# Kernel optimization log

Hardware: AMD Instinct MI355X
Metric: run time of the kernel (lower is better)

Reference implementation:

```python
import jax, jax.numpy as jnp
import numpy as np

B, L, C = 8, 256, 64
NEG = -1e30  # large negative instead of -inf to keep grads NaN-free


def setup_inputs() -> dict:
    key = jax.random.key(0)
    k1, k2 = jax.random.split(key)
    scores = jax.random.normal(k1, (B, L, L, C), dtype=jnp.float32)
    lens = jax.random.randint(k2, (B,), 64, L, dtype=jnp.int32)  # sentence lengths in [64, L-1]
    return {"scores": scores, "lens": lens}


def _inside_max(scores, lens):
    """Max-semiring CKY inside pass. scores: [B,L,L,C]; returns logZ per batch [B]."""
    t = jnp.transpose(jnp.max(scores, axis=-1), (1, 2, 0))  # [L,L,B] best label per span
    s0 = jnp.zeros((L, L, B), scores.dtype)                 # chart s[i,j] = best score of span (i,j)
    i = jnp.arange(L)
    j = jnp.arange(L)

    def step(s, w):
        e = jnp.clip(i + w, 0, L - 1)                       # span end, [L]
        k = jnp.clip(i[:, None] + j[None, :], 0, L - 1)     # split points, [L,L]
        left = s[i[:, None], k]                             # s[i, i+j], [L,L,B]
        right = s[k, e[:, None]]                            # s[i+j, i+w], [L,L,B]
        valid = (j[None, :] >= 1) & (j[None, :] < w) & ((i + w) < L)[:, None]
        comb = jnp.max(jnp.where(valid[..., None], left + right, NEG), axis=1)  # [L,B]
        s_l = t[i, e]                                       # label-max span score, [L,B]
        diag = jnp.where(w == 1, s_l, comb + s_l)
        row_ok = ((i + w) < L)[:, None]
        upd = jnp.where(row_ok, diag, s[i, e])
        s = s.at[i, e].set(upd)
        return s, None

    s, _ = jax.lax.scan(step, s0, jnp.arange(1, L))
    lens_c = jnp.clip(lens, 1, L - 1)
    return s[0, lens_c, jnp.arange(B)]                      # logZ (best tree score) per sentence


def reference(scores, lens):
    return _inside_max(scores, lens)
```

## Files before the change

kernel.cpp:

```cpp
#include <hip/hip_runtime.h>

#define LVAL 256
#define T    32
#define ST   36
#define SLAB (T * ST)
#define NB   8
#define NEG  (-1e30f)

typedef float f32x4 __attribute__((ext_vector_type(4)));

#define SOFT_FENCE() asm volatile("" ::: "memory")

__device__ __forceinline__ size_t sidx(int b, int i, int e) {
    return ((size_t)b << 16) + (i << 8) + e;
}

__device__ __forceinline__ void st_coh4(float* p, f32x4 v) {
    asm volatile("global_store_dwordx4 %0, %1, off sc0 sc1"
                 :: "v"(p), "v"(v) : "memory");
}
__device__ __forceinline__ f32x4 ld_coh4(const float* p) {
    f32x4 v;
    asm volatile("global_load_dwordx4 %0, %1, off sc0 sc1\n\t"
                 "s_waitcnt vmcnt(0)"
                 : "=&v"(v) : "v"(p) : "memory");
    return v;
}
__device__ __forceinline__ void ld_coh4x4(const float* p,
                                          f32x4& a, f32x4& b, f32x4& c, f32x4& d) {
    asm volatile("global_load_dwordx4 %0, %4, off sc0 sc1\n\t"
                 "global_load_dwordx4 %1, %4, off offset:16 sc0 sc1\n\t"
                 "global_load_dwordx4 %2, %4, off offset:32 sc0 sc1\n\t"
                 "global_load_dwordx4 %3, %4, off offset:48 sc0 sc1\n\t"
                 "s_waitcnt vmcnt(0)"
                 : "=&v"(a), "=&v"(b), "=&v"(c), "=&v"(d)
                 : "v"(p) : "memory");
}

template<int CTRL>
__device__ __forceinline__ float dpp_max(float v) {
#if __has_builtin(__builtin_amdgcn_mov_dpp)
    int o = __builtin_amdgcn_mov_dpp(__builtin_bit_cast(int, v), CTRL, 0xF, 0xF, true);
    return fmaxf(v, __builtin_bit_cast(float, o));
#else
    return fmaxf(v, __shfl_xor(v, CTRL == 0xB1 ? 1 : 2));
#endif
}

__global__ __launch_bounds__(256) void phase1(const float* __restrict__ scores,
                                              float* __restrict__ s,
                                              int* __restrict__ bar) {
    if (blockIdx.x == 0 && blockIdx.y == 0) {
        for (int k = threadIdx.x; k < 2048; k += 256) bar[k] = 0;
    }
    const int i = blockIdx.x, b = blockIdx.y;
    const int sub = threadIdx.x & 15, slot = threadIdx.x >> 4;
    const float* row = scores + ((((size_t)b * LVAL + i) * LVAL) << 6);
    #pragma unroll 4
    for (int m0 = 0; m0 < LVAL; m0 += 16) {
        const int e = m0 + slot;
        if (e > i) {
            float4 v = *((const float4*)(row + ((size_t)e << 6)) + sub);
            float mx = fmaxf(fmaxf(v.x, v.y), fmaxf(v.z, v.w));
            #pragma unroll
            for (int d = 1; d < 16; d <<= 1) mx = fmaxf(mx, __shfl_xor(mx, d));
            if (sub == 0) s[sidx(b, i, e)] = mx;
        }
    }
}

template<int LP>
__device__ __forceinline__ void diag_step(int lane, int l,
                                          float (*cur)[ST], float (*curT)[ST],
                                          const float (*tb)[ST]) {
    const int cells = T - l;
    const int P = 1 << LP;
    const int c = lane >> LP, p = lane & (P - 1);
    const bool guard = c < cells;
    const int li = guard ? c : 0;
    const int le = guard ? c + l : 0;
    constexpr int NF = 8 >> LP;
    const float tv = tb[li][le];
    float acc = NEG;
    #pragma unroll
    for (int m = 0; m < NF; ++m) {
        const int k0 = 4 * (p + m * P);
        float4 cu = *(const float4*)&cur[li][k0];
        float4 ct = *(const float4*)&curT[le][k0];
        acc = fmaxf(acc, fmaxf(fmaxf(cu.x + ct.x, cu.y + ct.y),
                               fmaxf(cu.z + ct.z, cu.w + ct.w)));
    }
    acc = dpp_max<0xB1>(acc);
    if (LP >= 2) acc = dpp_max<0x4E>(acc);
    const float v = acc + tv;
    if (guard && p == 0) cur[li][le] = v;
    if (guard && p == 1) curT[le][li] = v;
}

template<int LP>
__device__ __forceinline__ void edge_step(int lane, int l, int D,
                                          const float (*Ae)[ST], const float (*BeT)[ST],
                                          float (*cur)[ST], float (*curT)[ST],
                                          const float (*tb)[ST], const float (*pre)[ST]) {
    const int delta = l - (T - 1);
    const int ad = delta < 0 ? -delta : delta;
    const int cells = T - ad;
    const int P = 1 << LP;
    const int c = lane >> LP, p = lane & (P - 1);
    const bool guard = c < cells;
    const int li = guard ? (delta < 0 ? c + ad : c) : 0;
    const int le = guard ? li + delta : 0;
    constexpr int NF = 8 >> LP;
    const float tv = tb[li][le];
    float acc = pre[li][le];
    #pragma unroll
    for (int m = 0; m < NF; ++m) {
        const int k0 = 4 * (p + m * P);
        float4 a  = *(const float4*)&Ae[li][k0];
        float4 ct = *(const float4*)&curT[le][k0];
        float4 cu = *(const float4*)&cur[li][k0];
        float4 bt = *(const float4*)&BeT[le][k0];
        float s0 = fmaxf(fmaxf(a.x + ct.x, a.y + ct.y), fmaxf(a.z + ct.z, a.w + ct.w));
        float s1 = fmaxf(fmaxf(cu.x + bt.x, cu.y + bt.y), fmaxf(cu.z + bt.z, cu.w + bt.w));
        acc = fmaxf(acc, fmaxf(s0, s1));
    }
    acc = dpp_max<0xB1>(acc);
    if (LP >= 2) acc = dpp_max<0x4E>(acc);
    const float v = (D == 1 && l == 0) ? tv : acc + tv;
    if (guard && p == 0) cur[li][le] = v;
    if (guard && p == 1) curT[le][li] = v;
}

__device__ __forceinline__ void batch_barrier(int* __restrict__ bar, int b,
                                              int tid, int ep) {
    asm volatile("s_waitcnt vmcnt(0)" ::: "memory");
    __syncthreads();
    if (tid == 0) {
        int* cnt  = bar + b * 256;
        int* flag = bar + b * 256 + 64;
        int prev = __hip_atomic_fetch_add(cnt, 1, __ATOMIC_RELAXED,
                                          __HIP_MEMORY_SCOPE_AGENT);
        if ((prev & (NB - 1)) == NB - 1) {
            __hip_atomic_store(flag, ep, __ATOMIC_RELAXED, __HIP_MEMORY_SCOPE_AGENT);
        } else {
            int guard = 0;
            while (__hip_atomic_load(flag, __ATOMIC_RELAXED,
                                     __HIP_MEMORY_SCOPE_AGENT) < ep) {
                __builtin_amdgcn_s_sleep(2);
                if (++guard > (1 << 22)) break;
            }
        }
    }
    __syncthreads();
}

__global__ __launch_bounds__(256) void dp_fused(float* __restrict__ s,
                                                const int* __restrict__ lens,
                                                float* __restrict__ out,
                                                int* __restrict__ bar) {
    __shared__ __align__(16) float smem[14 * SLAB];
    float* ATb = smem;
    float (*Ae)[ST]  = (float(*)[ST])(smem + 6 * SLAB);
    float (*tb)[ST]  = (float(*)[ST])(smem + 7 * SLAB);
    float (*BeT)[ST] = (float(*)[ST])(smem + 8 * SLAB);
    float (*cur)[ST] = (float(*)[ST])(smem + 9 * SLAB);
    float* BWb = smem + 10 * SLAB;
    float (*pre)[ST] = (float(*)[ST])BWb;

    const int b  = blockIdx.x & 7;
    const int bi = blockIdx.x >> 3;
    const int tid = threadIdx.x, wid = tid >> 6, lane = tid & 63;
    const int lr = tid >> 5, lc = tid & 31;
    const int grow = lane >> 1, gc = (lane & 1) * 16;
    const int gly = lane >> 3, glx = lane & 7, r0 = 4 * gly, c0 = 4 * glx;
    const int trow = tid >> 3, tc4 = (tid & 7) * 4;
    float (*BW)[ST] = (float(*)[ST])(BWb + wid * SLAB);

    if (wid == 0) {
        float (*curT0)[ST] = (float(*)[ST])(BWb + 1 * SLAB);
        float (*t0)[ST]    = (float(*)[ST])(BWb + 2 * SLAB);
        const float4 negv = make_float4(NEG, NEG, NEG, NEG);
        #pragma unroll
        for (int j = 0; j < 4; ++j) {
            float4 v = *(const float4*)&s[sidx(b, bi * T + grow, bi * T + gc + 4 * j)];
            *(float4*)&t0[grow][gc + 4 * j]    = v;
            *(float4*)&Ae[grow][gc + 4 * j]    = negv;
            *(float4*)&curT0[grow][gc + 4 * j] = negv;
        }
        SOFT_FENCE();
        if (lane < T - 1) {
            float v = t0[lane][lane + 1];
            Ae[lane][lane + 1] = v;
            curT0[lane + 1][lane] = v;
        }
        SOFT_FENCE();
        #pragma unroll 1
        for (int l = 2; l < T; ++l) {
            if (T - l <= 16) diag_step<2>(lane, l, Ae, curT0, t0);
            else             diag_step<1>(lane, l, Ae, curT0, t0);
            SOFT_FENCE();
        }
        #pragma unroll
        for (int j = 0; j < 4; ++j)
            st_coh4(&s[sidx(b, bi * T + grow, bi * T + gc + 4 * j)],
                    *(const f32x4*)&Ae[grow][gc + 4 * j]);
    } else if (bi + 1 < NB) {
        for (int idx = tid - 64; idx < 256; idx += 192) {
            const int row = idx >> 3, c4 = (idx & 7) * 4;
            *(float4*)&tb[row][c4] =
                *(const float4*)&s[sidx(b, bi * T + row, (bi + 1) * T + c4)];
        }
    }

    #pragma unroll 1
    for (int D = 1; D < NB; ++D) {
        batch_barrier(bar, b, tid, D);
        const int be = bi + D;
        if (be < NB) {
            if (D == 1) {
                f32x4 v = ld_coh4(&s[sidx(b, be * T + trow, be * T + tc4)]);
                BeT[tc4 + 0][trow] = (trow < tc4 + 0) ? v[0] : NEG;
                BeT[tc4 + 1][trow] = (trow < tc4 + 1) ? v[1] : NEG;
                BeT[tc4 + 2][trow] = (trow < tc4 + 2) ? v[2] : NEG;
                BeT[tc4 + 3][trow] = (trow < tc4 + 3) ? v[3] : NEG;
            }
            const int nw = (D - 1 < 4) ? (D - 1) : 4;
            float ag[4][4];
            #pragma unroll
            for (int i = 0; i < 4; ++i)
                #pragma unroll
                for (int j = 0; j < 4; ++j) ag[i][j] = NEG;
            for (int K = bi + 1 + wid; K < be; K += 4) {
                const float (*AT)[ST] = (const float(*)[ST])(ATb + (K - bi - 1) * SLAB);
                f32x4 b0, b1, b2, b3;
                ld_coh4x4(&s[sidx(b, K * T + grow, be * T + gc)], b0, b1, b2, b3);
                *(f32x4*)&BW[grow][gc + 0]  = b0;
                *(f32x4*)&BW[grow][gc + 4]  = b1;
                *(f32x4*)&BW[grow][gc + 8]  = b2;
                *(f32x4*)&BW[grow][gc + 12] = b3;
                SOFT_FENCE();
                #pragma unroll 4
                for (int k = 0; k < T; ++k) {
                    float4 a4 = *(const float4*)&AT[k][r0];
                    float4 b4 = *(const float4*)&BW[k][c0];
                    const float aa[4] = {a4.x, a4.y, a4.z, a4.w};
                    const float bb[4] = {b4.x, b4.y, b4.z, b4.w};
                    #pragma unroll
                    for (int i = 0; i < 4; ++i)
                        #pragma unroll
                        for (int j = 0; j < 4; ++j)
                            ag[i][j] = fmaxf(ag[i][j], aa[i] + bb[j]);
                }
                SOFT_FENCE();
            }
            if (wid < nw) {
                #pragma unroll
                for (int i = 0; i < 4; ++i)
                    *(float4*)&BW[r0 + i][c0] =
                        make_float4(ag[i][0], ag[i][1], ag[i][2], ag[i][3]);
            }
            __syncthreads();
            #pragma unroll
            for (int r = 0; r < 4; ++r) {
                const int row = lr + 8 * r;
                float v = NEG;
                for (int w2 = 0; w2 < nw; ++w2)
                    v = fmaxf(v, BWb[w2 * SLAB + row * ST + lc]);
                pre[row][lc] = v;
            }
            __syncthreads();
            float (*curT)[ST] = (D == NB - 1) ? (float(*)[ST])(BWb + 1 * SLAB)
                                              : (float(*)[ST])(ATb + (D - 1) * SLAB);
            #pragma unroll
            for (int r = 0; r < 4; ++r) {
                const int row = lr + 8 * r;
                cur[row][lc]  = NEG;
                curT[row][lc] = NEG;
            }
            __syncthreads();
            if (wid == 0) {
                #pragma unroll 1
                for (int l = 0; l < 2 * T - 1; ++l) {
                    const int ad0 = (l < T - 1) ? (T - 1 - l) : (l - (T - 1));
                    if (ad0 >= 16) edge_step<2>(lane, l, D, Ae, BeT, cur, curT, tb, pre);
                    else           edge_step<1>(lane, l, D, Ae, BeT, cur, curT, tb, pre);
                    SOFT_FENCE();
                }
            }
            __syncthreads();
            {
                f32x4 pv = *(const f32x4*)&cur[trow][tc4];
                st_coh4(&s[sidx(b, bi * T + trow, be * T + tc4)], pv);
            }
            if (be + 1 < NB) {
                *(float4*)&tb[trow][tc4] =
                    *(const float4*)&s[sidx(b, bi * T + trow, (be + 1) * T + tc4)];
                f32x4 v = ld_coh4(&s[sidx(b, (be + 1) * T + trow,
                                          (be + 1) * T + tc4)]);
                BeT[tc4 + 0][trow] = (trow < tc4 + 0) ? v[0] : NEG;
                BeT[tc4 + 1][trow] = (trow < tc4 + 1) ? v[1] : NEG;
                BeT[tc4 + 2][trow] = (trow < tc4 + 2) ? v[2] : NEG;
                BeT[tc4 + 3][trow] = (trow < tc4 + 3) ? v[3] : NEG;
            }
        }
    }

    if (bi == 0 && tid == 0) {
        int len = lens[b];
        len = len < 1 ? 1 : (len > LVAL - 1 ? LVAL - 1 : len);
        const int K = len >> 5, off = len & 31;
        float r;
        if (K == 0)           r = Ae[0][off];
        else if (K == NB - 1) r = cur[0][off];
        else                  r = ATb[(K - 1) * SLAB + off * ST];
        out[b] = r;
    }
}

extern "C" void kernel_launch(void* const* d_in, const int* in_sizes, int n_in,
                              void* d_out, int out_size, void* d_ws, size_t ws_size,
                              hipStream_t stream) {
    const float* scores = (const float*)d_in[0];
    const int*   lens   = (const int*)d_in[1];
    float*       out    = (float*)d_out;
    float*       s      = (float*)d_ws;
    int*         bar    = (int*)((char*)d_ws + ((size_t)(8) << 16) * sizeof(float));

    phase1<<<dim3(LVAL, 8), 256, 0, stream>>>(scores, s, bar);
    dp_fused<<<64, 256, 0, stream>>>(s, lens, out, bar);
}
```

Measured before the change: 339.0 us.

## Software-pipeline wavefront diagonal steps with register forwarding of neighbor cells

Restructures the per-diagonal DP loops in the diagonal-block and edge-block wavefronts so that LDS operands for the next diagonal are loaded while the current one is computed. The dependency on the just-computed adjacent diagonal is handled by forwarding values through cross-lane shuffles instead of re-reading LDS. An opaque zero derived from the shuffled value orders the prefetch after the shuffle. Lane mapping is fixed at two lanes per cell, which drops the four-lane variant and raises register pressure. The loop over 2T edge steps now runs one extra iteration, which may write out-of-range cells or be inconsistent.

After: 359.8 us. 1.06x slower.

```diff
diff --git a/kernel.cpp b/kernel.cpp
--- a/kernel.cpp
+++ b/kernel.cpp
@@ -45,6 +45,26 @@
 #else
     return fmaxf(v, __shfl_xor(v, CTRL == 0xB1 ? 1 : 2));
 #endif
+}
+
+__device__ __forceinline__ int opaque_zero(float x) {
+    int z;
+    asm("v_and_b32 %0, 0, %1" : "=v"(z) : "v"(__float_as_int(x)));
+    return z;
+}
+
+__device__ __forceinline__ float red8(const f32x4 a, const f32x4 b,
+                                      const f32x4 c, const f32x4 d) {
+    float m0 = fmaxf(a.x + b.x, a.y + b.y);
+    float m1 = fmaxf(a.z + b.z, a.w + b.w);
+    float m2 = fmaxf(c.x + d.x, c.y + d.y);
+    float m3 = fmaxf(c.z + d.z, c.w + d.w);
+    return fmaxf(fmaxf(m0, m1), fmaxf(m2, m3));
+}
+__device__ __forceinline__ float red4(const f32x4 a, const f32x4 b) {
+    float m0 = fmaxf(a.x + b.x, a.y + b.y);
+    float m1 = fmaxf(a.z + b.z, a.w + b.w);
+    return fmaxf(m0, m1);
 }
 
 __global__ __launch_bounds__(256) void phase1(const float* __restrict__ scores,
@@ -69,66 +89,102 @@
     }
 }
 
-template<int LP>
-__device__ __forceinline__ void diag_step(int lane, int l,
-                                          float (*cur)[ST], float (*curT)[ST],
-                                          const float (*tb)[ST]) {
-    const int cells = T - l;
-    const int P = 1 << LP;
-    const int c = lane >> LP, p = lane & (P - 1);
-    const bool guard = c < cells;
-    const int li = guard ? c : 0;
-    const int le = guard ? c + l : 0;
-    constexpr int NF = 8 >> LP;
-    const float tv = tb[li][le];
-    float acc = NEG;
-    #pragma unroll
-    for (int m = 0; m < NF; ++m) {
-        const int k0 = 4 * (p + m * P);
-        float4 cu = *(const float4*)&cur[li][k0];
-        float4 ct = *(const float4*)&curT[le][k0];
-        acc = fmaxf(acc, fmaxf(fmaxf(cu.x + ct.x, cu.y + ct.y),
-                               fmaxf(cu.z + ct.z, cu.w + ct.w)));
-    }
-    acc = dpp_max<0xB1>(acc);
-    if (LP >= 2) acc = dpp_max<0x4E>(acc);
-    const float v = acc + tv;
-    if (guard && p == 0) cur[li][le] = v;
-    if (guard && p == 1) curT[le][li] = v;
-}
-
-template<int LP>
-__device__ __forceinline__ void edge_step(int lane, int l, int D,
-                                          const float (*Ae)[ST], const float (*BeT)[ST],
-                                          float (*cur)[ST], float (*curT)[ST],
-                                          const float (*tb)[ST], const float (*pre)[ST]) {
+struct EC {
+    f32x4 a[4], ct[4], cu[4], bt[4];
+    float tv, pr, afr, bfr;
+};
+
+__device__ __forceinline__ EC eprefetch(int l, int c, int p, int z,
+        const float (*Ae)[ST], const float (*BeT)[ST],
+        const float (*cur)[ST], const float (*curT)[ST],
+        const float (*tb)[ST], const float (*pre)[ST]) {
+    EC e;
     const int delta = l - (T - 1);
     const int ad = delta < 0 ? -delta : delta;
     const int cells = T - ad;
-    const int P = 1 << LP;
-    const int c = lane >> LP, p = lane & (P - 1);
-    const bool guard = c < cells;
-    const int li = guard ? (delta < 0 ? c + ad : c) : 0;
-    const int le = guard ? li + delta : 0;
-    constexpr int NF = 8 >> LP;
-    const float tv = tb[li][le];
-    float acc = pre[li][le];
+    const bool g = c < cells;
+    int li = g ? (delta < 0 ? c + ad : c) : 0;
+    int le = g ? li + delta : 0;
+    li += z; le += z;
+    e.tv  = tb[li][le];
+    e.pr  = pre[li][le];
+    e.afr = Ae[li][li + 1];
+    e.bfr = BeT[le][le > 0 ? le - 1 : 0];
     #pragma unroll
-    for (int m = 0; m < NF; ++m) {
-        const int k0 = 4 * (p + m * P);
-        float4 a  = *(const float4*)&Ae[li][k0];
-        float4 ct = *(const float4*)&curT[le][k0];
-        float4 cu = *(const float4*)&cur[li][k0];
-        float4 bt = *(const float4*)&BeT[le][k0];
-        float s0 = fmaxf(fmaxf(a.x + ct.x, a.y + ct.y), fmaxf(a.z + ct.z, a.w + ct.w));
-        float s1 = fmaxf(fmaxf(cu.x + bt.x, cu.y + bt.y), fmaxf(cu.z + bt.z, cu.w + bt.w));
-        acc = fmaxf(acc, fmaxf(s0, s1));
-    }
+    for (int m = 0; m < 4; ++m) {
+        const int k0 = 4 * (p + 2 * m);
+        e.a[m]  = *(const f32x4*)&Ae[li][k0];
+        e.ct[m] = *(const f32x4*)&curT[le][k0];
+        e.cu[m] = *(const f32x4*)&cur[li][k0];
+        e.bt[m] = *(const f32x4*)&BeT[le][k0];
+    }
+    return e;
+}
+
+__device__ __forceinline__ float ecompute(int l, int c, int p, int D,
+        const EC& e, float vprev, float vn,
+        float (*cur)[ST], float (*curT)[ST]) {
+    const int delta = l - (T - 1);
+    const int ad = delta < 0 ? -delta : delta;
+    const int cells = T - ad;
+    const bool g = c < cells;
+    const int li = g ? (delta < 0 ? c + ad : c) : 0;
+    const int le = g ? li + delta : 0;
+    const bool dpos = delta > 0;
+    float acc = e.pr;
+    #pragma unroll
+    for (int m = 0; m < 4; ++m)
+        acc = fmaxf(acc, red8(e.a[m], e.ct[m], e.cu[m], e.bt[m]));
+    const float srcL = dpos ? vn : vprev;
+    const float srcR = dpos ? vprev : vn;
+    const bool okL = dpos || (c != cells - 1);
+    const bool okR = dpos || (c != 0);
+    acc = fmaxf(acc, okL ? e.afr + srcL : NEG);
+    acc = fmaxf(acc, okR ? srcR + e.bfr : NEG);
     acc = dpp_max<0xB1>(acc);
-    if (LP >= 2) acc = dpp_max<0x4E>(acc);
-    const float v = (D == 1 && l == 0) ? tv : acc + tv;
-    if (guard && p == 0) cur[li][le] = v;
-    if (guard && p == 1) curT[le][li] = v;
+    const float v = (D == 1 && l == 0) ? e.tv : acc + e.tv;
+    if (g && p == 0) cur[li][le] = v;
+    if (g && p == 1) curT[le][li] = v;
+    return g ? v : NEG;
+}
+
+struct EC0 { f32x4 cu[4], ct[4]; float tvs, tfr; };
+
+__device__ __forceinline__ EC0 e0prefetch(int l, int c, int p, int z,
+        const float (*cur0)[ST], const float (*curT0)[ST], const float (*t0)[ST]) {
+    EC0 e;
+    const int cells = T - l;
+    const bool g = c < cells;
+    int li = c;
+    int le = g ? c + l : c;
+    li += z; le += z;
+    e.tvs = t0[li][le];
+    e.tfr = t0[le - 1][le];
+    #pragma unroll
+    for (int m = 0; m < 4; ++m) {
+        const int k0 = 4 * (p + 2 * m);
+        e.cu[m] = *(const f32x4*)&cur0[li][k0];
+        e.ct[m] = *(const f32x4*)&curT0[le][k0];
+    }
+    return e;
+}
+
+__device__ __forceinline__ float e0compute(int l, int c, int p,
+        const EC0& e, float vprev, float vn, float t0d,
+        float (*cur0)[ST], float (*curT0)[ST]) {
+    const int cells = T - l;
+    const bool g = c < cells;
+    const int li = c;
+    const int le = g ? c + l : c;
+    float acc = fmaxf(t0d + vn, vprev + e.tfr);
+    #pragma unroll
+    for (int m = 0; m < 4; ++m)
+        acc = fmaxf(acc, red4(e.cu[m], e.ct[m]));
+    acc = dpp_max<0xB1>(acc);
+    const float v = acc + e.tvs;
+    if (g && p == 0) cur0[li][le] = v;
+    if (g && p == 1) curT0[le][li] = v;
+    return g ? v : NEG;
 }
 
 __device__ __forceinline__ void batch_barrier(int* __restrict__ bar, int b,
@@ -175,6 +231,7 @@
     const int gly = lane >> 3, glx = lane & 7, r0 = 4 * gly, c0 = 4 * glx;
     const int trow = tid >> 3, tc4 = (tid & 7) * 4;
     float (*BW)[ST] = (float(*)[ST])(BWb + wid * SLAB);
+    const int c = lane >> 1, p = lane & 1;
 
     if (wid == 0) {
         float (*curT0)[ST] = (float(*)[ST])(BWb + 1 * SLAB);
@@ -194,11 +251,26 @@
             curT0[lane + 1][lane] = v;
         }
         SOFT_FENCE();
+        const float t0d = t0[c][c + 1];
+        float vprev = t0d;
+        EC0 fA = e0prefetch(2, c, p, 0, Ae, curT0, t0);
+        EC0 fB;
         #pragma unroll 1
-        for (int l = 2; l < T; ++l) {
-            if (T - l <= 16) diag_step<2>(lane, l, Ae, curT0, t0);
-            else             diag_step<1>(lane, l, Ae, curT0, t0);
-            SOFT_FENCE();
+        for (int l = 2; l < T; l += 2) {
+            {
+                float vn = __shfl(vprev, lane + 2);
+                int z = opaque_zero(vn);
+                fB = e0prefetch(l + 1, c, p, z, Ae, curT0, t0);
+                vprev = e0compute(l, c, p, fA, vprev, vn, t0d, Ae, curT0);
+                SOFT_FENCE();
+            }
+            {
+                float vn = __shfl(vprev, lane + 2);
+                int z = opaque_zero(vn);
+                if (l + 2 < T) fA = e0prefetch(l + 2, c, p, z, Ae, curT0, t0);
+                vprev = e0compute(l + 1, c, p, fB, vprev, vn, t0d, Ae, curT0);
+                SOFT_FENCE();
+            }
         }
         #pragma unroll
         for (int j = 0; j < 4; ++j)
@@ -279,12 +351,28 @@
             }
             __syncthreads();
             if (wid == 0) {
+                EC eA = eprefetch(0, c, p, 0, Ae, BeT, cur, curT, tb, pre);
+                EC eB;
+                float vprev = NEG;
                 #pragma unroll 1
-                for (int l = 0; l < 2 * T - 1; ++l) {
-                    const int ad0 = (l < T - 1) ? (T - 1 - l) : (l - (T - 1));
-                    if (ad0 >= 16) edge_step<2>(lane, l, D, Ae, BeT, cur, curT, tb, pre);
-                    else           edge_step<1>(lane, l, D, Ae, BeT, cur, curT, tb, pre);
-                    SOFT_FENCE();
+                for (int l = 0; l < 2 * T; l += 2) {
+                    {
+                        const bool dpos = (l > T - 1);
+                        float vn = __shfl(vprev, lane + (dpos ? 2 : -2));
+                        int z = opaque_zero(vn);
+                        eB = eprefetch(l + 1, c, p, z, Ae, BeT, cur, curT, tb, pre);
+                        vprev = ecompute(l, c, p, D, eA, vprev, vn, cur, curT);
+                        SOFT_FENCE();
+                    }
+                    {
+                        const bool dpos = (l + 1 > T - 1);
+                        float vn = __shfl(vprev, lane + (dpos ? 2 : -2));
+                        int z = opaque_zero(vn);
+                        if (l + 2 < 2 * T)
+                            eA = eprefetch(l + 2, c, p, z, Ae, BeT, cur, curT, tb, pre);
+                        vprev = ecompute(l + 1, c, p, D, eB, vprev, vn, cur, curT);
+                        SOFT_FENCE();
+                    }
                 }
             }
             __syncthreads();
```

## Prefetch next-step B tiles into registers while wave 0 runs edge sweep

Applied to the files above, without the earlier changes.

While wave 0 runs the serial diagonal edge sweep, waves 1-3 now prefetch the off-diagonal B tiles and the tb/BeT tiles for the next D step into registers, since those blocks are already final. At the next step the prefetched values go straight to LDS, and only wave 0 does a coherent global load for the freshly written block. This takes global load latency off the critical path after each barrier, at the cost of more register pressure and a fixed wave-to-tile assignment.

Measured after the change: 341.0 us. About the same (+0.6%).

```diff
diff --git a/kernel.cpp b/kernel.cpp
--- a/kernel.cpp
+++ b/kernel.cpp
@@ -131,6 +131,21 @@
     if (guard && p == 1) curT[le][li] = v;
 }
 
+__device__ __forceinline__ void gemm_blk(const float* ATs, const float (*BW)[ST],
+                                         int r0, int c0, float (&ag)[4][4]) {
+    const float (*AT)[ST] = (const float(*)[ST])ATs;
+    #pragma unroll 4
+    for (int k = 0; k < T; ++k) {
+        f32x4 a4 = *(const f32x4*)&AT[k][r0];
+        f32x4 b4 = *(const f32x4*)&BW[k][c0];
+        #pragma unroll
+        for (int i = 0; i < 4; ++i)
+            #pragma unroll
+            for (int j = 0; j < 4; ++j)
+                ag[i][j] = fmaxf(ag[i][j], a4[i] + b4[j]);
+    }
+}
+
 __device__ __forceinline__ void batch_barrier(int* __restrict__ bar, int b,
                                               int tid, int ep) {
     asm volatile("s_waitcnt vmcnt(0)" ::: "memory");
@@ -176,6 +191,9 @@
     const int trow = tid >> 3, tc4 = (tid & 7) * 4;
     float (*BW)[ST] = (float(*)[ST])(BWb + wid * SLAB);
 
+    f32x4 pbA[4], pbB[4];
+    f32x4 tpb[4], bpb[4];
+
     if (wid == 0) {
         float (*curT0)[ST] = (float(*)[ST])(BWb + 1 * SLAB);
         float (*t0)[ST]    = (float(*)[ST])(BWb + 2 * SLAB);
@@ -230,28 +248,34 @@
             for (int i = 0; i < 4; ++i)
                 #pragma unroll
                 for (int j = 0; j < 4; ++j) ag[i][j] = NEG;
-            for (int K = bi + 1 + wid; K < be; K += 4) {
-                const float (*AT)[ST] = (const float(*)[ST])(ATb + (K - bi - 1) * SLAB);
-                f32x4 b0, b1, b2, b3;
-                ld_coh4x4(&s[sidx(b, K * T + grow, be * T + gc)], b0, b1, b2, b3);
-                *(f32x4*)&BW[grow][gc + 0]  = b0;
-                *(f32x4*)&BW[grow][gc + 4]  = b1;
-                *(f32x4*)&BW[grow][gc + 8]  = b2;
-                *(f32x4*)&BW[grow][gc + 12] = b3;
-                SOFT_FENCE();
-                #pragma unroll 4
-                for (int k = 0; k < T; ++k) {
-                    float4 a4 = *(const float4*)&AT[k][r0];
-                    float4 b4 = *(const float4*)&BW[k][c0];
-                    const float aa[4] = {a4.x, a4.y, a4.z, a4.w};
-                    const float bb[4] = {b4.x, b4.y, b4.z, b4.w};
-                    #pragma unroll
-                    for (int i = 0; i < 4; ++i)
+            if (D >= 2) {
+                if (wid == 0) {
+                    f32x4 b0, b1, b2, b3;
+                    ld_coh4x4(&s[sidx(b, (bi + 1) * T + grow, be * T + gc)],
+                              b0, b1, b2, b3);
+                    *(f32x4*)&BW[grow][gc + 0]  = b0;
+                    *(f32x4*)&BW[grow][gc + 4]  = b1;
+                    *(f32x4*)&BW[grow][gc + 8]  = b2;
+                    *(f32x4*)&BW[grow][gc + 12] = b3;
+                    SOFT_FENCE();
+                    gemm_blk(ATb + 0, BW, r0, c0, ag);
+                } else {
+                    if (wid <= D - 2) {
                         #pragma unroll
                         for (int j = 0; j < 4; ++j)
-                            ag[i][j] = fmaxf(ag[i][j], aa[i] + bb[j]);
-                }
-                SOFT_FENCE();
+                            *(f32x4*)&BW[grow][gc + 4 * j] = pbA[j];
+                        SOFT_FENCE();
+                        gemm_blk(ATb + wid * SLAB, BW, r0, c0, ag);
+                        SOFT_FENCE();
+                    }
+                    if (wid + 3 <= D - 2) {
+                        #pragma unroll
+                        for (int j = 0; j < 4; ++j)
+                            *(f32x4*)&BW[grow][gc + 4 * j] = pbB[j];
+                        SOFT_FENCE();
+                        gemm_blk(ATb + (wid + 3) * SLAB, BW, r0, c0, ag);
+                    }
+                }
             }
             if (wid < nw) {
                 #pragma unroll
@@ -286,6 +310,25 @@
                     else           edge_step<1>(lane, l, D, Ae, BeT, cur, curT, tb, pre);
                     SOFT_FENCE();
                 }
+            } else if (be + 1 < NB) {
+                if (wid <= D - 1)
+                    ld_coh4x4(&s[sidx(b, (bi + 1 + wid) * T + grow, (be + 1) * T + gc)],
+                              pbA[0], pbA[1], pbA[2], pbA[3]);
+                if (wid + 3 <= D - 1)
+                    ld_coh4x4(&s[sidx(b, (bi + 4 + wid) * T + grow, (be + 1) * T + gc)],
+                              pbB[0], pbB[1], pbB[2], pbB[3]);
+                if (wid == 1) {
+                    #pragma unroll
+                    for (int j = 0; j < 4; ++j)
+                        tpb[j] = *(const f32x4*)&s[sidx(b, bi * T + grow,
+                                                        (be + 1) * T + gc + 4 * j)];
+                }
+                if (wid == 2) {
+                    #pragma unroll
+                    for (int j = 0; j < 4; ++j)
+                        bpb[j] = ld_coh4(&s[sidx(b, (be + 1) * T + grow,
+                                                 (be + 1) * T + gc + 4 * j)]);
+                }
             }
             __syncthreads();
             {
@@ -293,14 +336,20 @@
                 st_coh4(&s[sidx(b, bi * T + trow, be * T + tc4)], pv);
             }
             if (be + 1 < NB) {
-                *(float4*)&tb[trow][tc4] =
-                    *(const float4*)&s[sidx(b, bi * T + trow, (be + 1) * T + tc4)];
-                f32x4 v = ld_coh4(&s[sidx(b, (be + 1) * T + trow,
-                                          (be + 1) * T + tc4)]);
-                BeT[tc4 + 0][trow] = (trow < tc4 + 0) ? v[0] : NEG;
-                BeT[tc4 + 1][trow] = (trow < tc4 + 1) ? v[1] : NEG;
-                BeT[tc4 + 2][trow] = (trow < tc4 + 2) ? v[2] : NEG;
-                BeT[tc4 + 3][trow] = (trow < tc4 + 3) ? v[3] : NEG;
+                if (wid == 1) {
+                    #pragma unroll
+                    for (int j = 0; j < 4; ++j)
+                        *(f32x4*)&tb[grow][gc + 4 * j] = tpb[j];
+                }
+                if (wid == 2) {
+                    #pragma unroll
+                    for (int j = 0; j < 4; ++j)
+                        #pragma unroll
+                        for (int k = 0; k < 4; ++k) {
+                            const int col = gc + 4 * j + k;
+                            BeT[col][grow] = (grow < col) ? bpb[j][k] : NEG;
+                        }
+                }
             }
         }
     }
```
